# Kernel optimization log

Hardware: AMD Instinct MI355X
Metric: run time of the kernel (lower is better)

Reference implementation:

```python
import jax, jax.numpy as jnp
import numpy as np

N_NODES = 40000
N_EDGES = 320000
IN_C = 256
OUT_C = 256
K = 5


def setup_inputs() -> dict:
    key = jax.random.key(0)
    k1, k2, k3, k4, k5 = jax.random.split(key, 5)
    x = jax.random.normal(k1, (N_NODES, IN_C), dtype=jnp.float32)
    edge_index = jax.random.randint(k2, (2, N_EDGES), 0, N_NODES, dtype=jnp.int64)
    edge_weight = jax.random.uniform(k3, (N_EDGES,), dtype=jnp.float32)
    # parameters: uniform(-stdv, stdv) with stdv = 1/sqrt(in_channels * K)
    stdv = 1.0 / np.sqrt(IN_C * K)
    weight = jax.random.uniform(k4, (K, IN_C, OUT_C), dtype=jnp.float32,
                                minval=-stdv, maxval=stdv)
    bias = jax.random.uniform(k5, (OUT_C,), dtype=jnp.float32,
                              minval=-stdv, maxval=stdv)
    return {"x": x, "edge_index": edge_index, "edge_weight": edge_weight,
            "weight": weight, "bias": bias}


def reference(x, edge_index, edge_weight, weight, bias):
    row, col = edge_index[0], edge_index[1]
    num_nodes = x.shape[0]
    k_order = weight.shape[0]

    # remove_self_loops: mask out row==col edges (static-shape equivalent)
    keep = (row != col)
    ew = jnp.where(keep, edge_weight, 0.0)

    # degree over rows (counting only non-self-loop edges), D^{-1/2}
    deg = jax.ops.segment_sum(keep.astype(x.dtype), row, num_segments=num_nodes)
    deg_inv_sqrt = jnp.where(deg > 0, jax.lax.rsqrt(jnp.maximum(deg, 1.0)), 0.0)

    # scaled Laplacian edge values: -d_r^{-1/2} * w * d_c^{-1/2}
    lap = -deg_inv_sqrt[row] * ew * deg_inv_sqrt[col]

    def spmm(v):  # [N, C] -> [N, C] : scatter-add of lap-weighted gathered rows
        return jax.ops.segment_sum(lap[:, None] * v[col], row, num_segments=num_nodes)

    # Chebyshev recursion: T0 = x, T1 = L x, T_k = 2 L T_{k-1} - T_{k-2}
    tx0 = x
    out = tx0 @ weight[0]
    if k_order > 1:
        tx1 = spmm(x)
        out = out + tx1 @ weight[1]
        for k in range(2, k_order):
            tx2 = 2.0 * spmm(tx1) - tx0
            out = out + tx2 @ weight[k]
            tx0, tx1 = tx1, tx2
    return out + bias
```

## Files before the change

### kernel.cpp

```cpp
#include <hip/hip_runtime.h>

#define NN 40000
#define NE 320000
#define C 256
#define KORD 5
#define KT 1280

typedef __attribute__((ext_vector_type(8))) short short8;
typedef __attribute__((ext_vector_type(4))) float floatx4;
typedef unsigned short bf16_t;

__device__ __forceinline__ bf16_t f2bf(float f) {
    union { float f; unsigned u; } v; v.f = f;
    unsigned r = v.u + 0x7fffu + ((v.u >> 16) & 1u);
    return (bf16_t)(r >> 16);
}
__device__ __forceinline__ float bf2f(bf16_t h) {
    union { unsigned u; float f; } v; v.u = ((unsigned)h) << 16;
    return v.f;
}

#define GLL16(gsrc, ldst)                                                        \
    __builtin_amdgcn_global_load_lds(                                            \
        (const __attribute__((address_space(1))) void*)(gsrc),                   \
        (__attribute__((address_space(3))) void*)(ldst), 16, 0, 0)


__global__ void count_kernel(const int* __restrict__ ei,
                             int* __restrict__ deg_keep,
                             int* __restrict__ cnt_all) {
    int e = blockIdx.x * 256 + threadIdx.x;
    if (e >= NE) return;
    int r = ei[e];
    int c = ei[NE + e];
    atomicAdd(&cnt_all[r], 1);
    if (r != c) atomicAdd(&deg_keep[r], 1);
}

__global__ void dis_kernel(const int* __restrict__ deg, float* __restrict__ dis) {
    int n = blockIdx.x * 256 + threadIdx.x;
    if (n >= NN) return;
    int d = deg[n];
    dis[n] = (d > 0) ? rsqrtf((float)d) : 0.0f;
}

__global__ void scan1_kernel(const int* __restrict__ cnt,
                             int* __restrict__ incl,
                             int* __restrict__ bsum) {
    __shared__ int s[256];
    int t = threadIdx.x;
    int idx = blockIdx.x * 256 + t;
    int v = (idx < NN) ? cnt[idx] : 0;
    s[t] = v;
    __syncthreads();
    for (int off = 1; off < 256; off <<= 1) {
        int add = (t >= off) ? s[t - off] : 0;
        __syncthreads();
        s[t] += add;
        __syncthreads();
    }
    if (idx < NN) incl[idx] = s[t];
    if (t == 255) bsum[blockIdx.x] = s[255];
}

__global__ void scan2_kernel(int* __restrict__ bsum, int nb) {
    __shared__ int s[256];
    int t = threadIdx.x;
    int v = (t < nb) ? bsum[t] : 0;
    s[t] = v;
    __syncthreads();
    for (int off = 1; off < 256; off <<= 1) {
        int add = (t >= off) ? s[t - off] : 0;
        __syncthreads();
        s[t] += add;
        __syncthreads();
    }
    if (t < nb) bsum[t] = s[t] - v;
}

__global__ void scan3_kernel(const int* __restrict__ cnt,
                             const int* __restrict__ incl,
                             const int* __restrict__ bexcl,
                             int* __restrict__ row_ptr,
                             int* __restrict__ cursor) {
    int idx = blockIdx.x * 256 + threadIdx.x;
    if (idx == 0) row_ptr[NN] = NE;
    if (idx >= NN) return;
    int rp = incl[idx] - cnt[idx] + bexcl[blockIdx.x];
    row_ptr[idx] = rp;
    cursor[idx]  = rp;
}

__global__ void fill_kernel(const int* __restrict__ ei,
                            const float* __restrict__ ew,
                            const float* __restrict__ dis,
                            int* __restrict__ cursor,
                            int* __restrict__ csr_col,
                            float* __restrict__ csr_val) {
    int e = blockIdx.x * 256 + threadIdx.x;
    if (e >= NE) return;
    int r = ei[e];
    int c = ei[NE + e];
    int pos = atomicAdd(&cursor[r], 1);
    float w = (r != c) ? ew[e] : 0.0f;
    csr_col[pos] = c;
    csr_val[pos] = -dis[r] * w * dis[c];
}

__global__ void convx_kernel(const float* __restrict__ x, bf16_t* __restrict__ abf) {
    int i = blockIdx.x * 256 + threadIdx.x;
    if (i >= NN * 64) return;
    int n = i >> 6, cg = i & 63;
    float4 f = *(const float4*)&x[(size_t)n * C + cg * 4];
    ushort4 h;
    h.x = f2bf(f.x); h.y = f2bf(f.y); h.z = f2bf(f.z); h.w = f2bf(f.w);
    *(ushort4*)&abf[(size_t)n * KT + cg * 4] = h;
}

__global__ void wt_kernel(const float* __restrict__ W, bf16_t* __restrict__ WT) {
    int t = blockIdx.x * 256 + threadIdx.x;
    if (t >= 256 * KT) return;
    int n = t & 255, kt = t >> 8;
    WT[(size_t)n * KT + kt] = f2bf(W[(size_t)kt * 256 + n]);
}

__global__ __launch_bounds__(256)
void spmm_kernel(const bf16_t* __restrict__ Vb,
                 const bf16_t* __restrict__ subb,
                 const int* __restrict__ row_ptr,
                 const int* __restrict__ csr_col,
                 const float* __restrict__ csr_val,
                 bf16_t* __restrict__ outb,
                 float alpha, int use_sub) {
    int wave = __builtin_amdgcn_readfirstlane(threadIdx.x >> 6);
    int lane = threadIdx.x & 63;
    int n = blockIdx.x * 4 + wave;
    int j0 = row_ptr[n];
    int j1 = row_ptr[n + 1];
    int cb = lane * 4;
    float a0 = 0.f, a1 = 0.f, a2 = 0.f, a3 = 0.f;
    int j = j0;
    for (; j + 8 <= j1; j += 8) {
        int cc[8]; float ww[8]; ushort4 vv[8];
#pragma unroll
        for (int u = 0; u < 8; ++u) { cc[u] = csr_col[j + u]; ww[u] = csr_val[j + u]; }
#pragma unroll
        for (int u = 0; u < 8; ++u) vv[u] = *(const ushort4*)&Vb[(size_t)cc[u] * KT + cb];
#pragma unroll
        for (int u = 0; u < 8; ++u) {
            a0 += ww[u] * bf2f(vv[u].x); a1 += ww[u] * bf2f(vv[u].y);
            a2 += ww[u] * bf2f(vv[u].z); a3 += ww[u] * bf2f(vv[u].w);
        }
    }
    for (; j + 4 <= j1; j += 4) {
        int cc[4]; float ww[4]; ushort4 vv[4];
#pragma unroll
        for (int u = 0; u < 4; ++u) { cc[u] = csr_col[j + u]; ww[u] = csr_val[j + u]; }
#pragma unroll
        for (int u = 0; u < 4; ++u) vv[u] = *(const ushort4*)&Vb[(size_t)cc[u] * KT + cb];
#pragma unroll
        for (int u = 0; u < 4; ++u) {
            a0 += ww[u] * bf2f(vv[u].x); a1 += ww[u] * bf2f(vv[u].y);
            a2 += ww[u] * bf2f(vv[u].z); a3 += ww[u] * bf2f(vv[u].w);
        }
    }
    for (; j < j1; ++j) {
        int   col = csr_col[j];
        float w   = csr_val[j];
        ushort4 v = *(const ushort4*)&Vb[(size_t)col * KT + cb];
        a0 += w * bf2f(v.x); a1 += w * bf2f(v.y);
        a2 += w * bf2f(v.z); a3 += w * bf2f(v.w);
    }
    float r0, r1, r2, r3;
    if (use_sub) {
        ushort4 s = *(const ushort4*)&subb[(size_t)n * KT + cb];
        r0 = alpha * a0 - bf2f(s.x);
        r1 = alpha * a1 - bf2f(s.y);
        r2 = alpha * a2 - bf2f(s.z);
        r3 = alpha * a3 - bf2f(s.w);
    } else {
        r0 = alpha * a0; r1 = alpha * a1; r2 = alpha * a2; r3 = alpha * a3;
    }
    ushort4 h;
    h.x = f2bf(r0); h.y = f2bf(r1); h.z = f2bf(r2); h.w = f2bf(r3);
    *(ushort4*)&outb[(size_t)n * KT + cb] = h;
}

__global__ __launch_bounds__(256, 5)
void gemm_mfma(const bf16_t* __restrict__ Abf,
               const bf16_t* __restrict__ WT,
               const float* __restrict__ bias,
               float* __restrict__ out) {
    __shared__ bf16_t smem[12288];
    int tid = threadIdx.x;
    int w = tid >> 6, lane = tid & 63;
    int m0 = blockIdx.x * 64;
    int n0 = blockIdx.y * 128;
    int wm = w & 1, wn = w >> 1;
    int quad = lane >> 4, l16 = lane & 15, l7 = l16 & 7;

    const bf16_t* srcbase[6];
#pragma unroll
    for (int j = 0; j < 6; ++j) {
        int gi = (w * 6 + j) * 64 + lane;
        int isB = gi >= 512;
        int t  = isB ? gi - 512 : gi;
        int row = t >> 3;
        int pg = t & 7;
        int g  = pg ^ (row & 7);
        srcbase[j] = (isB ? WT + (size_t)(n0 + row) * KT
                          : Abf + (size_t)(m0 + row) * KT) + g * 8;
    }

    int arowb = wm * 32 + l16;
    int browb = wn * 64 + l16;

    floatx4 acc[2][4] = {};

    for (int k0 = 0; k0 < KT; k0 += 64) {
        __syncthreads();
#pragma unroll
        for (int j = 0; j < 6; ++j)
            GLL16(srcbase[j] + k0, &smem[(w * 6 + j) * 512]);
        __syncthreads();

#pragma unroll
        for (int c = 0; c < 2; ++c) {
            int gp   = (c * 4 + quad) ^ l7;
            int aoff = (arowb * 8 + gp) * 8;
            int boff = 4096 + (browb * 8 + gp) * 8;
            short8 af[2], bfr[4];
#pragma unroll
            for (int mt = 0; mt < 2; ++mt) af[mt]  = *(const short8*)&smem[aoff + mt * 1024];
#pragma unroll
            for (int nt = 0; nt < 4; ++nt) bfr[nt] = *(const short8*)&smem[boff + nt * 1024];
#pragma unroll
            for (int mt = 0; mt < 2; ++mt)
#pragma unroll
                for (int nt = 0; nt < 4; ++nt)
                    acc[mt][nt] = __builtin_amdgcn_mfma_f32_16x16x32_bf16(
                        af[mt], bfr[nt], acc[mt][nt], 0, 0, 0);
        }
    }

#pragma unroll
    for (int nt = 0; nt < 4; ++nt) {
        int n = n0 + wn * 64 + nt * 16 + l16;
        float bv = bias[n];
#pragma unroll
        for (int mt = 0; mt < 2; ++mt) {
            int mbase = m0 + wm * 32 + mt * 16 + quad * 4;
#pragma unroll
            for (int r = 0; r < 4; ++r)
                out[(size_t)(mbase + r) * C + n] = acc[mt][nt][r] + bv;
        }
    }
}


extern "C" void kernel_launch(void* const* d_in, const int* in_sizes, int n_in,
                              void* d_out, int out_size, void* d_ws, size_t ws_size,
                              hipStream_t stream) {
    const float* x    = (const float*)d_in[0];
    const int*   ei   = (const int*)d_in[1];
    const float* ew   = (const float*)d_in[2];
    const float* W    = (const float*)d_in[3];
    const float* bias = (const float*)d_in[4];
    float* out = (float*)d_out;

    char* p = (char*)d_ws;
    auto carve = [&](size_t bytes) {
        char* q = p;
        p += (bytes + 255) & ~(size_t)255;
        return q;
    };
    int*    deg     = (int*)   carve(NN * 4);
    int*    cnt     = (int*)   carve(NN * 4);
    int*    incl    = (int*)   carve(NN * 4);
    int*    bsum    = (int*)   carve(256 * 4);
    int*    row_ptr = (int*)   carve((NN + 1) * 4);
    int*    cursor  = (int*)   carve(NN * 4);
    int*    csr_col = (int*)   carve(NE * 4);
    float*  csr_val = (float*) carve(NE * 4);
    float*  dis     = (float*) carve(NN * 4);
    bf16_t* abf     = (bf16_t*)carve((size_t)NN * KT * 2);
    bf16_t* WT      = (bf16_t*)carve((size_t)C * KT * 2);
    (void)ws_size; (void)n_in; (void)in_sizes; (void)out_size;

    const int NB_E = (NE + 255) / 256;
    const int NB_N = (NN + 255) / 256;

    hipMemsetAsync(deg, 0, NN * 4, stream);
    hipMemsetAsync(cnt, 0, NN * 4, stream);

    count_kernel<<<NB_E, 256, 0, stream>>>(ei, deg, cnt);
    dis_kernel<<<NB_N, 256, 0, stream>>>(deg, dis);
    scan1_kernel<<<NB_N, 256, 0, stream>>>(cnt, incl, bsum);
    scan2_kernel<<<1, 256, 0, stream>>>(bsum, NB_N);
    scan3_kernel<<<NB_N, 256, 0, stream>>>(cnt, incl, bsum, row_ptr, cursor);
    fill_kernel<<<NB_E, 256, 0, stream>>>(ei, ew, dis, cursor, csr_col, csr_val);

    convx_kernel<<<(NN * 64 + 255) / 256, 256, 0, stream>>>(x, abf);
    wt_kernel<<<(256 * KT + 255) / 256, 256, 0, stream>>>(W, WT);

    spmm_kernel<<<NN / 4, 256, 0, stream>>>(abf + 0 * 256, nullptr, row_ptr, csr_col,
                                            csr_val, abf + 1 * 256, 1.0f, 0);
    spmm_kernel<<<NN / 4, 256, 0, stream>>>(abf + 1 * 256, abf + 0 * 256, row_ptr,
                                            csr_col, csr_val, abf + 2 * 256, 2.0f, 1);
    spmm_kernel<<<NN / 4, 256, 0, stream>>>(abf + 2 * 256, abf + 1 * 256, row_ptr,
                                            csr_col, csr_val, abf + 3 * 256, 2.0f, 1);
    spmm_kernel<<<NN / 4, 256, 0, stream>>>(abf + 3 * 256, abf + 2 * 256, row_ptr,
                                            csr_col, csr_val, abf + 4 * 256, 2.0f, 1);

    dim3 ggrid(625, 2);
    gemm_mfma<<<ggrid, 256, 0, stream>>>(abf, WT, bias, out);
}
```

Before: 306.7 us.

## Store Chebyshev basis in blocked tile layout and use full-N GEMM tiles

Replaces the row-major [N, 1280] bf16 basis with a blocked layout. Each group of 64 nodes holds twenty contiguous 64x64 k-chunks, so every GEMM A-tile load is one contiguous 8KB region. The GEMM now computes all 256 output columns per block (64x256 tiles, 625 blocks) instead of splitting N across two blocks, which halves how often A is read. The cost is more LDS and accumulator registers, with occupancy lowered from 5 to 4. SpMM gathers now read 4 scattered 128B segments per node row instead of one 512B contiguous row, which may hurt gather efficiency.

```diff
diff --git a/kernel.cpp b/kernel.cpp
--- a/kernel.cpp
+++ b/kernel.cpp
@@ -18,6 +18,9 @@
 __device__ __forceinline__ float bf2f(bf16_t h) {
     union { unsigned u; float f; } v; v.u = ((unsigned)h) << 16;
     return v.f;
+}
+__device__ __forceinline__ size_t fnode(int n) {
+    return (size_t)(n >> 6) * 81920 + (size_t)(n & 63) * 64;
 }
 
 #define GLL16(gsrc, ldst)                                                        \
@@ -114,7 +117,7 @@
     float4 f = *(const float4*)&x[(size_t)n * C + cg * 4];
     ushort4 h;
     h.x = f2bf(f.x); h.y = f2bf(f.y); h.z = f2bf(f.z); h.w = f2bf(f.w);
-    *(ushort4*)&abf[(size_t)n * KT + cg * 4] = h;
+    *(ushort4*)&abf[fnode(n) + (size_t)(cg >> 4) * 4096 + (cg & 15) * 4] = h;
 }
 
 __global__ void wt_kernel(const float* __restrict__ W, bf16_t* __restrict__ WT) {
@@ -125,19 +128,18 @@
 }
 
 __global__ __launch_bounds__(256)
-void spmm_kernel(const bf16_t* __restrict__ Vb,
-                 const bf16_t* __restrict__ subb,
+void spmm_kernel(bf16_t* __restrict__ st,
                  const int* __restrict__ row_ptr,
                  const int* __restrict__ csr_col,
                  const float* __restrict__ csr_val,
-                 bf16_t* __restrict__ outb,
-                 float alpha, int use_sub) {
+                 float alpha, int kin, int kout, int ksub) {
     int wave = __builtin_amdgcn_readfirstlane(threadIdx.x >> 6);
     int lane = threadIdx.x & 63;
     int n = blockIdx.x * 4 + wave;
     int j0 = row_ptr[n];
     int j1 = row_ptr[n + 1];
-    int cb = lane * 4;
+    size_t lo = (size_t)(lane >> 4) * 4096 + (lane & 15) * 4;
+    const bf16_t* Vb = st + (size_t)kin * 16384;
     float a0 = 0.f, a1 = 0.f, a2 = 0.f, a3 = 0.f;
     int j = j0;
     for (; j + 8 <= j1; j += 8) {
@@ -145,7 +147,7 @@
 #pragma unroll
         for (int u = 0; u < 8; ++u) { cc[u] = csr_col[j + u]; ww[u] = csr_val[j + u]; }
 #pragma unroll
-        for (int u = 0; u < 8; ++u) vv[u] = *(const ushort4*)&Vb[(size_t)cc[u] * KT + cb];
+        for (int u = 0; u < 8; ++u) vv[u] = *(const ushort4*)&Vb[fnode(cc[u]) + lo];
 #pragma unroll
         for (int u = 0; u < 8; ++u) {
             a0 += ww[u] * bf2f(vv[u].x); a1 += ww[u] * bf2f(vv[u].y);
@@ -157,7 +159,7 @@
 #pragma unroll
         for (int u = 0; u < 4; ++u) { cc[u] = csr_col[j + u]; ww[u] = csr_val[j + u]; }
 #pragma unroll
-        for (int u = 0; u < 4; ++u) vv[u] = *(const ushort4*)&Vb[(size_t)cc[u] * KT + cb];
+        for (int u = 0; u < 4; ++u) vv[u] = *(const ushort4*)&Vb[fnode(cc[u]) + lo];
 #pragma unroll
         for (int u = 0; u < 4; ++u) {
             a0 += ww[u] * bf2f(vv[u].x); a1 += ww[u] * bf2f(vv[u].y);
@@ -167,13 +169,13 @@
     for (; j < j1; ++j) {
         int   col = csr_col[j];
         float w   = csr_val[j];
-        ushort4 v = *(const ushort4*)&Vb[(size_t)col * KT + cb];
+        ushort4 v = *(const ushort4*)&Vb[fnode(col) + lo];
         a0 += w * bf2f(v.x); a1 += w * bf2f(v.y);
         a2 += w * bf2f(v.z); a3 += w * bf2f(v.w);
     }
     float r0, r1, r2, r3;
-    if (use_sub) {
-        ushort4 s = *(const ushort4*)&subb[(size_t)n * KT + cb];
+    if (ksub >= 0) {
+        ushort4 s = *(const ushort4*)&st[(size_t)ksub * 16384 + fnode(n) + lo];
         r0 = alpha * a0 - bf2f(s.x);
         r1 = alpha * a1 - bf2f(s.y);
         r2 = alpha * a2 - bf2f(s.z);
@@ -183,59 +185,59 @@
     }
     ushort4 h;
     h.x = f2bf(r0); h.y = f2bf(r1); h.z = f2bf(r2); h.w = f2bf(r3);
-    *(ushort4*)&outb[(size_t)n * KT + cb] = h;
-}
-
-__global__ __launch_bounds__(256, 5)
-void gemm_mfma(const bf16_t* __restrict__ Abf,
+    *(ushort4*)&st[(size_t)kout * 16384 + fnode(n) + lo] = h;
+}
+
+__global__ __launch_bounds__(256, 4)
+void gemm_mfma(const bf16_t* __restrict__ ABlk,
                const bf16_t* __restrict__ WT,
                const float* __restrict__ bias,
                float* __restrict__ out) {
-    __shared__ bf16_t smem[12288];
+    __shared__ bf16_t smem[20480];
     int tid = threadIdx.x;
     int w = tid >> 6, lane = tid & 63;
-    int m0 = blockIdx.x * 64;
-    int n0 = blockIdx.y * 128;
-    int wm = w & 1, wn = w >> 1;
+    int p = blockIdx.x;
+    int m0 = p * 64;
     int quad = lane >> 4, l16 = lane & 15, l7 = l16 & 7;
 
-    const bf16_t* srcbase[6];
-#pragma unroll
-    for (int j = 0; j < 6; ++j) {
-        int gi = (w * 6 + j) * 64 + lane;
-        int isB = gi >= 512;
-        int t  = isB ? gi - 512 : gi;
+    const bf16_t* srcbase[10];
+    int strd[10];
+#pragma unroll
+    for (int j = 0; j < 10; ++j) {
+        int gi = (w * 10 + j) * 64 + lane;
+        int isA = gi < 512;
+        int t  = isA ? gi : gi - 512;
         int row = t >> 3;
         int pg = t & 7;
         int g  = pg ^ (row & 7);
-        srcbase[j] = (isB ? WT + (size_t)(n0 + row) * KT
-                          : Abf + (size_t)(m0 + row) * KT) + g * 8;
-    }
-
-    int arowb = wm * 32 + l16;
-    int browb = wn * 64 + l16;
-
-    floatx4 acc[2][4] = {};
-
-    for (int k0 = 0; k0 < KT; k0 += 64) {
-        __syncthreads();
-#pragma unroll
-        for (int j = 0; j < 6; ++j)
-            GLL16(srcbase[j] + k0, &smem[(w * 6 + j) * 512]);
+        srcbase[j] = isA ? ABlk + (size_t)p * 81920 + (row * 8 + g) * 8
+                         : WT + (size_t)row * KT + g * 8;
+        strd[j] = isA ? 4096 : 64;
+    }
+
+    int browb = w * 64 + l16;
+
+    floatx4 acc[4][4] = {};
+
+    for (int ki = 0; ki < 20; ++ki) {
+        __syncthreads();
+#pragma unroll
+        for (int j = 0; j < 10; ++j)
+            GLL16(srcbase[j] + (size_t)ki * strd[j], &smem[(w * 10 + j) * 512]);
         __syncthreads();
 
 #pragma unroll
         for (int c = 0; c < 2; ++c) {
             int gp   = (c * 4 + quad) ^ l7;
-            int aoff = (arowb * 8 + gp) * 8;
+            int aoff = (l16 * 8 + gp) * 8;
             int boff = 4096 + (browb * 8 + gp) * 8;
-            short8 af[2], bfr[4];
-#pragma unroll
-            for (int mt = 0; mt < 2; ++mt) af[mt]  = *(const short8*)&smem[aoff + mt * 1024];
+            short8 af[4], bfr[4];
+#pragma unroll
+            for (int mt = 0; mt < 4; ++mt) af[mt]  = *(const short8*)&smem[aoff + mt * 1024];
 #pragma unroll
             for (int nt = 0; nt < 4; ++nt) bfr[nt] = *(const short8*)&smem[boff + nt * 1024];
 #pragma unroll
-            for (int mt = 0; mt < 2; ++mt)
+            for (int mt = 0; mt < 4; ++mt)
 #pragma unroll
                 for (int nt = 0; nt < 4; ++nt)
                     acc[mt][nt] = __builtin_amdgcn_mfma_f32_16x16x32_bf16(
@@ -245,11 +247,11 @@
 
 #pragma unroll
     for (int nt = 0; nt < 4; ++nt) {
-        int n = n0 + wn * 64 + nt * 16 + l16;
+        int n = w * 64 + nt * 16 + l16;
         float bv = bias[n];
 #pragma unroll
-        for (int mt = 0; mt < 2; ++mt) {
-            int mbase = m0 + wm * 32 + mt * 16 + quad * 4;
+        for (int mt = 0; mt < 4; ++mt) {
+            int mbase = m0 + mt * 16 + quad * 4;
 #pragma unroll
             for (int r = 0; r < 4; ++r)
                 out[(size_t)(mbase + r) * C + n] = acc[mt][nt][r] + bv;
@@ -303,15 +305,14 @@
     convx_kernel<<<(NN * 64 + 255) / 256, 256, 0, stream>>>(x, abf);
     wt_kernel<<<(256 * KT + 255) / 256, 256, 0, stream>>>(W, WT);
 
-    spmm_kernel<<<NN / 4, 256, 0, stream>>>(abf + 0 * 256, nullptr, row_ptr, csr_col,
-                                            csr_val, abf + 1 * 256, 1.0f, 0);
-    spmm_kernel<<<NN / 4, 256, 0, stream>>>(abf + 1 * 256, abf + 0 * 256, row_ptr,
-                                            csr_col, csr_val, abf + 2 * 256, 2.0f, 1);
-    spmm_kernel<<<NN / 4, 256, 0, stream>>>(abf + 2 * 256, abf + 1 * 256, row_ptr,
-                                            csr_col, csr_val, abf + 3 * 256, 2.0f, 1);
-    spmm_kernel<<<NN / 4, 256, 0, stream>>>(abf + 3 * 256, abf + 2 * 256, row_ptr,
-                                            csr_col, csr_val, abf + 4 * 256, 2.0f, 1);
-
-    dim3 ggrid(625, 2);
-    gemm_mfma<<<ggrid, 256, 0, stream>>>(abf, WT, bias, out);
-}
+    spmm_kernel<<<NN / 4, 256, 0, stream>>>(abf, row_ptr, csr_col, csr_val,
+                                            1.0f, 0, 1, -1);
+    spmm_kernel<<<NN / 4, 256, 0, stream>>>(abf, row_ptr, csr_col, csr_val,
+                                            2.0f, 1, 2, 0);
+    spmm_kernel<<<NN / 4, 256, 0, stream>>>(abf, row_ptr, csr_col, csr_val,
+                                            2.0f, 2, 3, 1);
+    spmm_kernel<<<NN / 4, 256, 0, stream>>>(abf, row_ptr, csr_col, csr_val,
+                                            2.0f, 3, 4, 2);
+
+    gemm_mfma<<<625, 256, 0, stream>>>(abf, WT, bias, out);
+}
```

New measurement: 327.2 us. 1.07x slower.
